# Kernel optimization log

Hardware: AMD Instinct MI355X
Metric: run time of the kernel (lower is better)

Reference implementation:

```python
import jax, jax.numpy as jnp
import numpy as np

N = 30000          # nodes
DEG = 16           # in-degree per node
E = N * DEG        # edges per etype
T = 3              # edge types
IN = 128           # in_feats
HID = 256          # hidden_size
HEADS = 4
CLS = 2            # num_classes
NEG_SLOPE = 0.2    # DGL GATConv default


def setup_inputs() -> dict:
    key = jax.random.key(0)
    ks = jax.random.split(key, 14)
    s = lambda k, shape: (jax.random.normal(k, shape, jnp.float32) * 0.05)
    feat = jax.random.normal(ks[0], (N, IN), jnp.float32)
    src = jax.random.randint(ks[1], (T, E), 0, N)
    # every node gets exactly DEG incoming edges per etype (DGL forbids 0-in-degree)
    dst = jnp.tile(jnp.repeat(jnp.arange(N), DEG), (T, 1))
    D = HID // HEADS
    return {
        "feat": feat,
        "W0": s(ks[2], (T, IN, HID)),  "al0": s(ks[3], (T, HEADS, D)), "ar0": s(ks[4], (T, HEADS, D)), "b0": jnp.zeros((T, HID), jnp.float32),
        "W1": s(ks[5], (T, HID, HID)), "al1": s(ks[6], (T, HEADS, D)), "ar1": s(ks[7], (T, HEADS, D)), "b1": jnp.zeros((T, HID), jnp.float32),
        "W2": s(ks[8], (T, HID, CLS)), "al2": s(ks[9], (T, 1, CLS)),   "ar2": s(ks[10], (T, 1, CLS)), "b2": jnp.zeros((T, CLS), jnp.float32),
        "src": src, "dst": dst,
    }


def _gat(feat, W, al, ar, b, src, dst):
    """DGL GATConv: feat [n,F], W [F,H*D], al/ar [H,D], b [H*D] -> [n,H,D]."""
    n = feat.shape[0]
    H, D = al.shape
    h = (feat @ W).reshape(n, H, D)                      # projected features
    el = jnp.sum(h * al, axis=-1)                        # [n,H]
    er = jnp.sum(h * ar, axis=-1)                        # [n,H]
    e = jax.nn.leaky_relu(el[src] + er[dst], NEG_SLOPE)  # [E,H] edge scores
    # segment softmax over incoming edges of each dst node
    emax = jax.ops.segment_max(e, dst, num_segments=n)
    ex = jnp.exp(e - emax[dst])
    den = jax.ops.segment_sum(ex, dst, num_segments=n)
    alpha = ex / den[dst]                                # [E,H]
    out = jax.ops.segment_sum(h[src] * alpha[:, :, None], dst, num_segments=n)
    return out + b.reshape(H, D)


def _hetero(feat, W, al, ar, b, src, dst):
    # HeteroGraphConv(aggregate='mean') over T edge types on one node type
    outs = [_gat(feat, W[t], al[t], ar[t], b[t], src[t], dst[t]) for t in range(W.shape[0])]
    return jnp.mean(jnp.stack(outs, 0), axis=0)


def reference(feat, W0, al0, ar0, b0, W1, al1, ar1, b1, W2, al2, ar2, b2, src, dst):
    h = jax.nn.elu(_hetero(feat, W0, al0, ar0, b0, src, dst).reshape(N, -1))
    h = jax.nn.elu(_hetero(h, W1, al1, ar1, b1, src, dst).reshape(N, -1))
    logits = _hetero(h, W2, al2, ar2, b2, src, dst)      # [N,1,CLS]
    # faithful to F.softmax(logits[primary_ntype], dim=1): dim=1 is the size-1 head axis
    return logits, jax.nn.softmax(logits, axis=1)
```

## Files before the change

kernel.cpp:

```cpp
#include <hip/hip_runtime.h>
#include <hip/hip_bf16.h>
#include <hip/hip_fp8.h>
#include <math.h>

#define N_NODES 30000
#define DEG     16
#define NE      480000
#define NT      3
#define IN_F    128
#define HID_F   256
#define HEADS   4
#define DH      64
#define CLS     2
#define SLOPE   0.2f

#define NTILES      1875
#define NTILES_AL   1880
#define KC0         4
#define KC1         8

typedef __hip_bfloat16 bf16;
typedef __attribute__((ext_vector_type(8))) short short8;
typedef __attribute__((ext_vector_type(4))) float floatx4;

__device__ __forceinline__ float bf2f(short x) {
    unsigned int u = ((unsigned int)(unsigned short)x) << 16;
    float f;
    __builtin_memcpy(&f, &u, 4);
    return f;
}
__device__ __forceinline__ short f2bf_s(float x) {
    bf16 b = bf16(x);
    short s;
    __builtin_memcpy(&s, &b, 2);
    return s;
}

__device__ __forceinline__ void fp8x4_decode(unsigned int u, float* f) {
#if __has_builtin(__builtin_amdgcn_cvt_pk_f32_fp8)
    auto lo = __builtin_amdgcn_cvt_pk_f32_fp8((int)u, false);
    auto hi = __builtin_amdgcn_cvt_pk_f32_fp8((int)u, true);
    f[0] = lo[0]; f[1] = lo[1]; f[2] = hi[0]; f[3] = hi[1];
#else
#pragma unroll
    for (int j = 0; j < 4; j++) {
        __hip_fp8_e4m3 q;
        q.__x = (unsigned char)((u >> (8 * j)) & 0xff);
        f[j] = (float)q;
    }
#endif
}
__device__ __forceinline__ unsigned int fp8_encode4_u32(float v0, float v1,
                                                        float v2, float v3) {
#if __has_builtin(__builtin_amdgcn_cvt_pk_fp8_f32)
    int p01 = __builtin_amdgcn_cvt_pk_fp8_f32(v0, v1, 0, false);
    int p23 = __builtin_amdgcn_cvt_pk_fp8_f32(v2, v3, 0, false);
    return ((unsigned int)p01 & 0xffffu) | ((unsigned int)p23 << 16);
#else
    __hip_fp8_e4m3 q0(v0), q1(v1), q2(v2), q3(v3);
    return (unsigned int)q0.__x | ((unsigned int)q1.__x << 8) |
           ((unsigned int)q2.__x << 16) | ((unsigned int)q3.__x << 24);
#endif
}


#define APACK_THREADS (N_NODES * (IN_F / 8))
#define BP0_THREADS   (NT * 16 * KC0 * 64)
#define BP1_THREADS   (NT * 16 * KC1 * 64)
__global__ void prep(const float* __restrict__ feat, const float* __restrict__ W0,
                     const float* __restrict__ W1, short* __restrict__ Apack0,
                     short* __restrict__ Bpack0, short* __restrict__ Bpack1) {
    int g = blockIdx.x * 256 + threadIdx.x;
    if (g < APACK_THREADS) {
        int row = g >> 4, j8 = g & 15;
        int k0 = j8 * 8;
        const float* src = feat + (size_t)row * IN_F + k0;
        int ntile = row >> 4, C = k0 >> 5, quad = (k0 >> 3) & 3;
        int lane  = (row & 15) + 16 * quad;
        short* dst = Apack0 + ((size_t)(ntile * KC0 + C) * 64 + lane) * 8;
        short8 o;
#pragma unroll
        for (int j = 0; j < 8; j++) o[j] = f2bf_s(src[j]);
        *(short8*)dst = o;
        return;
    }
    g -= APACK_THREADS;
    if (g < BP0_THREADS) {
        int t = g / (16 * KC0 * 64), rem = g % (16 * KC0 * 64);
        int nt = rem / (KC0 * 64);
        int C  = (rem / 64) % KC0;
        int lane = rem & 63, l15 = lane & 15, quad = lane >> 4;
        int col = nt * 16 + l15, k0 = C * 32 + quad * 8;
        const float* src = W0 + (size_t)t * IN_F * HID_F + (size_t)k0 * HID_F + col;
        short* dst = Bpack0 + ((size_t)t * 16 * KC0 + nt * KC0 + C) * 512 + lane * 8;
        short8 o;
#pragma unroll
        for (int j = 0; j < 8; j++) o[j] = f2bf_s(src[(size_t)j * HID_F]);
        *(short8*)dst = o;
        return;
    }
    g -= BP0_THREADS;
    if (g < BP1_THREADS) {
        int t = g / (16 * KC1 * 64), rem = g % (16 * KC1 * 64);
        int nt = rem / (KC1 * 64);
        int C  = (rem / 64) % KC1;
        int lane = rem & 63, l15 = lane & 15, quad = lane >> 4;
        int col = nt * 16 + l15, k0 = C * 32 + quad * 8;
        const float* src = W1 + (size_t)t * HID_F * HID_F + (size_t)k0 * HID_F + col;
        short* dst = Bpack1 + ((size_t)t * 16 * KC1 + nt * KC1 + C) * 512 + lane * 8;
        short8 o;
#pragma unroll
        for (int j = 0; j < 8; j++) o[j] = f2bf_s(src[(size_t)j * HID_F]);
        *(short8*)dst = o;
    }
}

template <int K>
__global__ __launch_bounds__(256, 4) void gemm_proj(const short* __restrict__ Apack,
                                                    const short* __restrict__ Bpack,
                                                    const float* __restrict__ al,
                                                    const float* __restrict__ ar,
                                                    unsigned char* __restrict__ Hout,
                                                    float* __restrict__ el,
                                                    float* __restrict__ er) {
    const int KC = K / 32;
    int nh   = blockIdx.y;
    int t    = blockIdx.z;
    int tid  = threadIdx.x;
    int wave = tid >> 6, lane = tid & 63;
    int quad = lane >> 4, l15 = lane & 15;
    int e0   = blockIdx.x * 8 + wave * 2;

    const short* Ap0 = Apack + (size_t)(e0)     * KC * 512 + lane * 8;
    const short* Ap1 = Apack + (size_t)(e0 + 1) * KC * 512 + lane * 8;
    const short* Bp  = Bpack + ((size_t)t * 16 + nh * 8) * KC * 512 + lane * 8;
    unsigned char* Ht = Hout + (size_t)t * N_NODES * HID_F;

    floatx4 acc[8][2];
#pragma unroll
    for (int i = 0; i < 8; i++) {
        acc[i][0] = (floatx4){0.f, 0.f, 0.f, 0.f};
        acc[i][1] = (floatx4){0.f, 0.f, 0.f, 0.f};
    }

#pragma unroll
    for (int C = 0; C < KC; C++) {
        short8 xb0 = *(const short8*)(Ap0 + (size_t)C * 512);
        short8 xb1 = *(const short8*)(Ap1 + (size_t)C * 512);
#pragma unroll
        for (int nt = 0; nt < 8; nt++) {
            short8 wa = *(const short8*)(Bp + (size_t)(nt * KC + C) * 512);
            acc[nt][0] = __builtin_amdgcn_mfma_f32_16x16x32_bf16(wa, xb0, acc[nt][0], 0, 0, 0);
            acc[nt][1] = __builtin_amdgcn_mfma_f32_16x16x32_bf16(wa, xb1, acc[nt][1], 0, 0, 0);
        }
    }

#pragma unroll
    for (int e = 0; e < 2; e++) {
        int node = (e0 + e) * 16 + l15;
        bool ok  = node < N_NODES;
#pragma unroll
        for (int nt = 0; nt < 8; nt++) {
            unsigned int u = fp8_encode4_u32(acc[nt][e][0], acc[nt][e][1],
                                             acc[nt][e][2], acc[nt][e][3]);
            if (ok)
                *(unsigned int*)(Ht + (size_t)node * HID_F + (nh * 8 + nt) * 16 + quad * 4) = u;
        }
#pragma unroll
        for (int hl = 0; hl < 2; hl++) {
            int h = nh * 2 + hl;
            float pl = 0.f, pr = 0.f;
#pragma unroll
            for (int j = 0; j < 4; j++) {
                int nt = hl * 4 + j;
                int coff = t * HID_F + (nh * 8 + nt) * 16 + quad * 4;
                float4 av = *(const float4*)(al + coff);
                float4 rv = *(const float4*)(ar + coff);
                pl += acc[nt][e][0] * av.x + acc[nt][e][1] * av.y +
                      acc[nt][e][2] * av.z + acc[nt][e][3] * av.w;
                pr += acc[nt][e][0] * rv.x + acc[nt][e][1] * rv.y +
                      acc[nt][e][2] * rv.z + acc[nt][e][3] * rv.w;
            }
            pl += __shfl_xor(pl, 16); pl += __shfl_xor(pl, 32);
            pr += __shfl_xor(pr, 16); pr += __shfl_xor(pr, 32);
            if (lane < 16 && ok) {
                el[((size_t)t * N_NODES + node) * HEADS + h] = pl;
                er[((size_t)t * N_NODES + node) * HEADS + h] = pr;
            }
        }
    }
}

template <bool PACK>
__global__ __launch_bounds__(256) void gat_agg(const unsigned char* __restrict__ Hproj,
                                               const float* __restrict__ el,
                                               const float* __restrict__ er,
                                               const int* __restrict__ src,
                                               const float* __restrict__ bias,
                                               short* __restrict__ out) {
    int blk = blockIdx.x;
    int tid = threadIdx.x;
    __shared__ int   s_src[8][NT][DEG];
    __shared__ float s_w[8][NT][HEADS][DEG];

#pragma unroll
    for (int it = 0; it < 2; it++) {
        int j = it * 256 + tid;
        if (j < NT * 128) {
            int t = j / 128, k = j % 128;
            s_src[k >> 4][t][k & 15] = src[(size_t)t * NE + blk * 128 + k];
        }
    }
    __syncthreads();

    {
        int lane16 = tid & 15;
        int ubase  = tid >> 4;
#pragma unroll
        for (int it = 0; it < 6; it++) {
            int u = it * 16 + ubase;
            int g = u / 12, rem = u % 12;
            int t = rem >> 2, h = rem & 3;
            int n = blk * 8 + g;
            int s = s_src[g][t][lane16];
            float e = el[((size_t)t * N_NODES + s) * HEADS + h] +
                      er[((size_t)t * N_NODES + n) * HEADS + h];
            e = e > 0.f ? e : SLOPE * e;
            float m = e;
            m = fmaxf(m, __shfl_xor(m, 1));
            m = fmaxf(m, __shfl_xor(m, 2));
            m = fmaxf(m, __shfl_xor(m, 4));
            m = fmaxf(m, __shfl_xor(m, 8));
            float p = __expf(e - m);
            float ss = p;
            ss += __shfl_xor(ss, 1);
            ss += __shfl_xor(ss, 2);
            ss += __shfl_xor(ss, 4);
            ss += __shfl_xor(ss, 8);
            s_w[g][t][h][lane16] = p / ss;
        }
    }
    __syncthreads();

    int g = tid >> 5, c = tid & 31;
    int n = blk * 8 + g;
    int h = c >> 3;
    int col0 = c * 8;

    float acc[8];
#pragma unroll
    for (int j = 0; j < 8; j++) acc[j] = 0.f;

#pragma unroll
    for (int t = 0; t < NT; t++) {
        const unsigned char* Hh = Hproj + (size_t)t * N_NODES * HID_F;
#pragma unroll
        for (int i = 0; i < DEG; i++) {
            int s   = s_src[g][t][i];
            float w = s_w[g][t][h][i];
            uint2 v = *(const uint2*)(Hh + (size_t)s * HID_F + col0);
            float f[8];
            fp8x4_decode(v.x, f);
            fp8x4_decode(v.y, f + 4);
#pragma unroll
            for (int j = 0; j < 8; j++) acc[j] += w * f[j];
        }
    }

    short8 o;
#pragma unroll
    for (int j = 0; j < 8; j++) {
        float bsum = bias[0 * HID_F + col0 + j] + bias[1 * HID_F + col0 + j] +
                     bias[2 * HID_F + col0 + j];
        float res = (acc[j] + bsum) * (1.f / 3.f);
        res = res > 0.f ? res : (__expf(res) - 1.f);
        o[j] = f2bf_s(res);
    }
    if (PACK) {
        int ntile = n >> 4, kc = c >> 2, quad = c & 3;
        int lane  = (n & 15) + 16 * quad;
        *(short8*)(out + ((size_t)(ntile * KC1 + kc) * 64 + lane) * 8) = o;
    } else {
        *(short8*)(out + (size_t)n * HID_F + col0) = o;
    }
}

__global__ __launch_bounds__(256) void proj2(const short* __restrict__ X,
                                             const float* __restrict__ W2,
                                             const float* __restrict__ al2,
                                             const float* __restrict__ ar2,
                                             float* __restrict__ p2,
                                             float* __restrict__ el2,
                                             float* __restrict__ er2) {
    int n    = blockIdx.x * 4 + (threadIdx.x >> 6);
    int lane = threadIdx.x & 63;
    const short* Xr = X + (size_t)n * HID_F + lane * 4;
    float x[4];
    x[0] = bf2f(Xr[0]); x[1] = bf2f(Xr[1]); x[2] = bf2f(Xr[2]); x[3] = bf2f(Xr[3]);
    float a[NT][CLS];
#pragma unroll
    for (int t = 0; t < NT; t++)
#pragma unroll
        for (int cc = 0; cc < CLS; cc++) {
            float v = 0.f;
#pragma unroll
            for (int j = 0; j < 4; j++)
                v += x[j] * W2[(size_t)t * HID_F * CLS + (lane * 4 + j) * CLS + cc];
#pragma unroll
            for (int off = 32; off; off >>= 1) v += __shfl_xor(v, off);
            a[t][cc] = v;
        }
    if (lane == 0) {
#pragma unroll
        for (int t = 0; t < NT; t++) {
            p2[((size_t)t * N_NODES + n) * CLS + 0] = a[t][0];
            p2[((size_t)t * N_NODES + n) * CLS + 1] = a[t][1];
            el2[(size_t)t * N_NODES + n] = a[t][0] * al2[t * CLS + 0] + a[t][1] * al2[t * CLS + 1];
            er2[(size_t)t * N_NODES + n] = a[t][0] * ar2[t * CLS + 0] + a[t][1] * ar2[t * CLS + 1];
        }
    }
}

__global__ void final_layer(const float* __restrict__ p2,
                            const float* __restrict__ el2,
                            const float* __restrict__ er2,
                            const int* __restrict__ src,
                            const float* __restrict__ b2,
                            float* __restrict__ out) {
    int n = blockIdx.x * 256 + threadIdx.x;
    if (n >= N_NODES) return;
    float l0 = 0.f, l1 = 0.f;
    for (int t = 0; t < NT; t++) {
        float erv = er2[(size_t)t * N_NODES + n];
        const int* sp = src + (size_t)t * NE + n * DEG;
        float ev[DEG];
        float m = -1e30f;
#pragma unroll
        for (int i = 0; i < DEG; i++) {
            int s   = sp[i];
            float e = el2[(size_t)t * N_NODES + s] + erv;
            e = e > 0.f ? e : SLOPE * e;
            ev[i] = e;
            m = fmaxf(m, e);
        }
        float den = 0.f, a0 = 0.f, a1 = 0.f;
#pragma unroll
        for (int i = 0; i < DEG; i++) {
            int s   = sp[i];
            float p = __expf(ev[i] - m);
            den += p;
            a0  += p * p2[((size_t)t * N_NODES + s) * CLS + 0];
            a1  += p * p2[((size_t)t * N_NODES + s) * CLS + 1];
        }
        l0 += a0 / den + b2[t * CLS + 0];
        l1 += a1 / den + b2[t * CLS + 1];
    }
    l0 *= (1.f / 3.f);
    l1 *= (1.f / 3.f);
    out[(size_t)n * CLS + 0] = l0;
    out[(size_t)n * CLS + 1] = l1;
    float* out2 = out + (size_t)N_NODES * CLS;
    out2[(size_t)n * CLS + 0] = 1.0f;
    out2[(size_t)n * CLS + 1] = 1.0f;
}

extern "C" void kernel_launch(void* const* d_in, const int* in_sizes, int n_in,
                              void* d_out, int out_size, void* d_ws, size_t ws_size,
                              hipStream_t stream) {
    const float* feat = (const float*)d_in[0];
    const float* W0   = (const float*)d_in[1];
    const float* al0  = (const float*)d_in[2];
    const float* ar0  = (const float*)d_in[3];
    const float* b0   = (const float*)d_in[4];
    const float* W1   = (const float*)d_in[5];
    const float* al1  = (const float*)d_in[6];
    const float* ar1  = (const float*)d_in[7];
    const float* b1   = (const float*)d_in[8];
    const float* W2   = (const float*)d_in[9];
    const float* al2  = (const float*)d_in[10];
    const float* ar2  = (const float*)d_in[11];
    const float* b2   = (const float*)d_in[12];
    const int*   src  = (const int*)d_in[13];

    char* w = (char*)d_ws;
    auto alloc = [&](size_t bytes) {
        char* p = w;
        w += (bytes + 255) & ~(size_t)255;
        return p;
    };
    short* Apack0 = (short*)alloc((size_t)NTILES_AL * KC0 * 512 * 2);
    short* Apack1 = (short*)alloc((size_t)NTILES_AL * KC1 * 512 * 2);
    short* Bpack0 = (short*)alloc((size_t)NT * 16 * KC0 * 512 * 2);
    short* Bpack1 = (short*)alloc((size_t)NT * 16 * KC1 * 512 * 2);
    unsigned char* Hproj = (unsigned char*)alloc((size_t)NT * N_NODES * HID_F);
    short* h2    = (short*)alloc((size_t)N_NODES * HID_F * 2);
    float* el    = (float*)alloc((size_t)NT * N_NODES * HEADS * 4);
    float* er    = (float*)alloc((size_t)NT * N_NODES * HEADS * 4);
    float* p2    = (float*)alloc((size_t)NT * N_NODES * CLS * 4);
    float* el2   = (float*)alloc((size_t)NT * N_NODES * 4);
    float* er2   = (float*)alloc((size_t)NT * N_NODES * 4);

    int prep_total = APACK_THREADS + BP0_THREADS + BP1_THREADS;
    prep<<<(prep_total + 255) / 256, 256, 0, stream>>>(feat, W0, W1, Apack0,
                                                       Bpack0, Bpack1);

    dim3 ggrid((NTILES + 7) / 8, 2, NT);

    gemm_proj<IN_F><<<ggrid, 256, 0, stream>>>(Apack0, Bpack0, al0, ar0, Hproj, el, er);
    gat_agg<true><<<N_NODES / 8, 256, 0, stream>>>(Hproj, el, er, src, b0, Apack1);

    gemm_proj<HID_F><<<ggrid, 256, 0, stream>>>(Apack1, Bpack1, al1, ar1, Hproj, el, er);
    gat_agg<false><<<N_NODES / 8, 256, 0, stream>>>(Hproj, el, er, src, b1, h2);

    proj2<<<dim3(N_NODES / 4), 256, 0, stream>>>(h2, W2, al2, ar2, p2, el2, er2);
    final_layer<<<(N_NODES + 255) / 256, 256, 0, stream>>>(p2, el2, er2, src, b2,
                                                           (float*)d_out);
}
```

Baseline: 322.0 us.

## Slice projected features into 32-column planes and aggregate per slice

The fp8 projected feature matrix is stored as 8 column slices of 32 bytes per node instead of 256-byte rows. Each aggregation block now handles 64 nodes for a single slice and single head, with padded shared memory. This shrinks the gather working set per slice so it fits in cache and gives better reuse across the random source indices. The cost is that softmax weights and source indices are recomputed in every slice block, roughly 8x redundant work on that part.

```diff
diff --git a/kernel.cpp b/kernel.cpp
--- a/kernel.cpp
+++ b/kernel.cpp
@@ -18,6 +18,8 @@
 #define NTILES_AL   1880
 #define KC0         4
 #define KC1         8
+#define NSLICE      8
+#define SW          17
 
 typedef __hip_bfloat16 bf16;
 typedef __attribute__((ext_vector_type(8))) short short8;
@@ -161,10 +163,12 @@
         bool ok  = node < N_NODES;
 #pragma unroll
         for (int nt = 0; nt < 8; nt++) {
+            int T = nh * 8 + nt;
             unsigned int u = fp8_encode4_u32(acc[nt][e][0], acc[nt][e][1],
                                              acc[nt][e][2], acc[nt][e][3]);
             if (ok)
-                *(unsigned int*)(Ht + (size_t)node * HID_F + (nh * 8 + nt) * 16 + quad * 4) = u;
+                *(unsigned int*)(Ht + ((size_t)(T >> 1) * N_NODES + node) * 32 +
+                                 (T & 1) * 16 + quad * 4) = u;
         }
 #pragma unroll
         for (int hl = 0; hl < 2; hl++) {
@@ -198,33 +202,37 @@
                                                const int* __restrict__ src,
                                                const float* __restrict__ bias,
                                                short* __restrict__ out) {
-    int blk = blockIdx.x;
-    int tid = threadIdx.x;
-    __shared__ int   s_src[8][NT][DEG];
-    __shared__ float s_w[8][NT][HEADS][DEG];
-
-#pragma unroll
-    for (int it = 0; it < 2; it++) {
+    int slice = blockIdx.x & 7;
+    int base  = (blockIdx.x >> 3) * 64;
+    int tid   = threadIdx.x;
+    int h     = slice >> 1;
+
+    __shared__ int   s_src[64 * NT * SW];
+    __shared__ float s_w[64 * NT * SW];
+
+#pragma unroll
+    for (int it = 0; it < 12; it++) {
         int j = it * 256 + tid;
-        if (j < NT * 128) {
-            int t = j / 128, k = j % 128;
-            s_src[k >> 4][t][k & 15] = src[(size_t)t * NE + blk * 128 + k];
-        }
+        int t = j >> 10, k = j & 1023;
+        int e = base * 16 + k;
+        int s = (e < NE) ? src[(size_t)t * NE + e] : 0;
+        s_src[((k >> 4) * NT + t) * SW + (k & 15)] = s;
     }
     __syncthreads();
 
     {
         int lane16 = tid & 15;
-        int ubase  = tid >> 4;
-#pragma unroll
-        for (int it = 0; it < 6; it++) {
-            int u = it * 16 + ubase;
-            int g = u / 12, rem = u % 12;
-            int t = rem >> 2, h = rem & 3;
-            int n = blk * 8 + g;
-            int s = s_src[g][t][lane16];
-            float e = el[((size_t)t * N_NODES + s) * HEADS + h] +
-                      er[((size_t)t * N_NODES + n) * HEADS + h];
+        int ub     = tid >> 4;
+#pragma unroll
+        for (int it = 0; it < 12; it++) {
+            int u  = it * 16 + ub;
+            int nl = u / 3, t = u % 3;
+            int n  = base + nl;
+            int s  = s_src[(nl * NT + t) * SW + lane16];
+            float e = 0.f;
+            if (n < N_NODES)
+                e = el[((size_t)t * N_NODES + s) * HEADS + h] +
+                    er[((size_t)t * N_NODES + n) * HEADS + h];
             e = e > 0.f ? e : SLOPE * e;
             float m = e;
             m = fmaxf(m, __shfl_xor(m, 1));
@@ -237,15 +245,13 @@
             ss += __shfl_xor(ss, 2);
             ss += __shfl_xor(ss, 4);
             ss += __shfl_xor(ss, 8);
-            s_w[g][t][h][lane16] = p / ss;
+            s_w[(nl * NT + t) * SW + lane16] = p / ss;
         }
     }
     __syncthreads();
 
-    int g = tid >> 5, c = tid & 31;
-    int n = blk * 8 + g;
-    int h = c >> 3;
-    int col0 = c * 8;
+    int nl = tid >> 2, q = tid & 3;
+    int n  = base + nl;
 
     float acc[8];
 #pragma unroll
@@ -253,12 +259,15 @@
 
 #pragma unroll
     for (int t = 0; t < NT; t++) {
-        const unsigned char* Hh = Hproj + (size_t)t * N_NODES * HID_F;
+        const unsigned char* Hh = Hproj +
+            ((size_t)t * NSLICE + slice) * N_NODES * 32 + q * 8;
+        const int*   sp = s_src + (nl * NT + t) * SW;
+        const float* wp = s_w   + (nl * NT + t) * SW;
 #pragma unroll
         for (int i = 0; i < DEG; i++) {
-            int s   = s_src[g][t][i];
-            float w = s_w[g][t][h][i];
-            uint2 v = *(const uint2*)(Hh + (size_t)s * HID_F + col0);
+            int s   = sp[i];
+            float w = wp[i];
+            uint2 v = *(const uint2*)(Hh + (size_t)s * 32);
             float f[8];
             fp8x4_decode(v.x, f);
             fp8x4_decode(v.y, f + 4);
@@ -267,6 +276,8 @@
         }
     }
 
+    if (n >= N_NODES) return;
+    int col0 = slice * 32 + q * 8;
     short8 o;
 #pragma unroll
     for (int j = 0; j < 8; j++) {
@@ -277,9 +288,9 @@
         o[j] = f2bf_s(res);
     }
     if (PACK) {
-        int ntile = n >> 4, kc = c >> 2, quad = c & 3;
-        int lane  = (n & 15) + 16 * quad;
-        *(short8*)(out + ((size_t)(ntile * KC1 + kc) * 64 + lane) * 8) = o;
+        int ntile = n >> 4;
+        *(short8*)(out + ((size_t)(ntile * KC1 + slice) * 64 +
+                          (n & 15) + 16 * q) * 8) = o;
     } else {
         *(short8*)(out + (size_t)n * HID_F + col0) = o;
     }
@@ -405,12 +416,13 @@
                                                        Bpack0, Bpack1);
 
     dim3 ggrid((NTILES + 7) / 8, 2, NT);
+    int  agrid = ((N_NODES + 63) / 64) * NSLICE;
 
     gemm_proj<IN_F><<<ggrid, 256, 0, stream>>>(Apack0, Bpack0, al0, ar0, Hproj, el, er);
-    gat_agg<true><<<N_NODES / 8, 256, 0, stream>>>(Hproj, el, er, src, b0, Apack1);
+    gat_agg<true><<<agrid, 256, 0, stream>>>(Hproj, el, er, src, b0, Apack1);
 
     gemm_proj<HID_F><<<ggrid, 256, 0, stream>>>(Apack1, Bpack1, al1, ar1, Hproj, el, er);
-    gat_agg<false><<<N_NODES / 8, 256, 0, stream>>>(Hproj, el, er, src, b1, h2);
+    gat_agg<false><<<agrid, 256, 0, stream>>>(Hproj, el, er, src, b1, h2);
 
     proj2<<<dim3(N_NODES / 4), 256, 0, stream>>>(h2, W2, al2, ar2, p2, el2, er2);
     final_layer<<<(N_NODES + 255) / 256, 256, 0, stream>>>(p2, el2, er2, src, b2,
```

Measured after the change: 433.3 us. +34.6%, slower.
